# Kernel optimization log

Hardware: AMD Instinct MI355X
Metric: run time of the kernel (lower is better)

Reference implementation:

```python
import jax, jax.numpy as jnp
import numpy as np

WH, WW = 16, 16            # window size
NUM_HEADS = 8


def _relative_position_index(wh, ww):
    ch = jnp.arange(wh)
    cw = jnp.arange(ww)
    coords = jnp.stack(jnp.meshgrid(ch, cw, indexing='ij'))        # [2, wh, ww]
    coords = coords.reshape(2, -1)                                  # [2, N]
    rel = coords[:, :, None] - coords[:, None, :]                   # [2, N, N]
    rel = rel.transpose(1, 2, 0)                                    # [N, N, 2]
    idx = (rel[..., 0] + wh - 1) * (2 * ww - 1) + (rel[..., 1] + ww - 1)
    return idx                                                      # [N, N] int32


def setup_inputs() -> dict:
    key = jax.random.key(0)
    ks = jax.random.split(key, 7)
    B, N, C = 128, WH * WW, 512
    x = jax.random.normal(ks[0], (B, N, C), dtype=jnp.float32)
    y = jax.random.normal(ks[1], (B, N, C), dtype=jnp.float32)
    # Linear weights stored as [in, out]; init ~ standard scale
    q_w = jax.random.normal(ks[2], (C, C), dtype=jnp.float32) * (C ** -0.5)
    kv_w = jax.random.normal(ks[3], (C, 2 * C), dtype=jnp.float32) * (C ** -0.5)
    proj_w = jax.random.normal(ks[4], (C, C), dtype=jnp.float32) * (C ** -0.5)
    proj_b = jax.random.normal(ks[5], (C,), dtype=jnp.float32) * 0.01
    n_rel = (2 * WH - 1) * (2 * WW - 1)  # 961
    bias_table = jax.random.normal(ks[6], (n_rel, NUM_HEADS), dtype=jnp.float32) * 0.02
    return {"x": x, "y": y, "q_w": q_w, "kv_w": kv_w,
            "proj_w": proj_w, "proj_b": proj_b, "bias_table": bias_table}


def reference(x, y, q_w, kv_w, proj_w, proj_b, bias_table):
    B, N1, C = x.shape
    _, N2, _ = y.shape
    H = NUM_HEADS
    d = C // H
    scale = d ** -0.5

    q = (x @ q_w).reshape(B, N1, H, d).transpose(0, 2, 1, 3)        # [B,H,N1,d]
    kv = (y @ kv_w).reshape(B, N2, 2, H, d)
    k = kv[:, :, 0].transpose(0, 2, 1, 3)                           # [B,H,N2,d]
    v = kv[:, :, 1].transpose(0, 2, 1, 3)                           # [B,H,N2,d]

    attn = jnp.einsum('bhqd,bhkd->bhqk', q, k) * scale              # [B,H,N1,N2]

    idx = _relative_position_index(WH, WW)                          # [N, N]
    rel_bias = bias_table[idx.reshape(-1)].reshape(N1, N2, H)       # gather
    rel_bias = rel_bias.transpose(2, 0, 1)                          # [H,N1,N2]
    attn = attn + rel_bias[None]

    attn = jax.nn.softmax(attn, axis=-1)
    out = jnp.einsum('bhqk,bhkd->bhqd', attn, v)                    # [B,H,N1,d]
    out = out.transpose(0, 2, 1, 3).reshape(B, N1, C)
    out = out @ proj_w + proj_b
    return out
```

## Files before the change

kernel.cpp:

```cpp
#include <hip/hip_runtime.h>

typedef unsigned short u16;
typedef __attribute__((ext_vector_type(8))) short short8;
typedef __attribute__((ext_vector_type(4))) float floatx4;

__device__ __forceinline__ float bf2f(u16 v){
  union { unsigned int u; float f; } x; x.u = ((unsigned int)v) << 16; return x.f;
}
__device__ __forceinline__ u16 f2bf(float f){
  union { float f; unsigned int u; } x; x.f = f;
  unsigned int r = x.u + 0x7FFFu + ((x.u >> 16) & 1u);
  return (u16)(r >> 16);
}
__device__ __forceinline__ short8 cvt8(float4 f0, float4 f1){
  short8 v;
  v[0] = (short)f2bf(f0.x); v[1] = (short)f2bf(f0.y);
  v[2] = (short)f2bf(f0.z); v[3] = (short)f2bf(f0.w);
  v[4] = (short)f2bf(f1.x); v[5] = (short)f2bf(f1.y);
  v[6] = (short)f2bf(f1.z); v[7] = (short)f2bf(f1.w);
  return v;
}

__device__ __forceinline__ void async16(const void* g, void* l){
  __builtin_amdgcn_global_load_lds(
      (__attribute__((address_space(1))) unsigned int*)const_cast<void*>(g),
      (__attribute__((address_space(3))) unsigned int*)l, 16, 0, 0);
}

__global__ __launch_bounds__(256)
void conv_bf16(const float* __restrict__ in, u16* __restrict__ out, int n8){
  const int stride = gridDim.x * 256;
  for (int i = blockIdx.x * 256 + threadIdx.x; i < n8; i += stride){
    float4 f0 = ((const float4*)in)[(size_t)i * 2];
    float4 f1 = ((const float4*)in)[(size_t)i * 2 + 1];
    *(short8*)(out + (size_t)i * 8) = cvt8(f0, f1);
  }
}

__global__ void transpose_f32(const float* __restrict__ in, u16* __restrict__ out,
                              int R, int C){
  __shared__ u16 t[32][33];
  const int tx = threadIdx.x;
  const int c0 = blockIdx.x * 32, r0 = blockIdx.y * 32;
  for (int i = tx; i < 1024; i += 256){
    int r = i >> 5, c = i & 31;
    t[r][c] = f2bf(in[(size_t)(r0 + r) * C + c0 + c]);
  }
  __syncthreads();
  for (int i = tx; i < 1024; i += 256){
    int r = i >> 5, c = i & 31;
    out[(size_t)(c0 + r) * R + r0 + c] = t[c][r];
  }
}

__global__ void bias_expand(const float* __restrict__ table, u16* __restrict__ Bm){
  int i = blockIdx.x * 256 + threadIdx.x;
  int q = i >> 8, k = i & 255;
  int rh = (q >> 4) - (k >> 4) + 15;
  int rw = (q & 15) - (k & 15) + 15;
  int idx = rh * 31 + rw;
  #pragma unroll
  for (int h = 0; h < 8; h++) Bm[h * 65536 + i] = f2bf(table[(size_t)idx * 8 + h]);
}

template<int MODE, int GX>
__global__ __launch_bounds__(512, 2)
void gemm_bt(const u16* __restrict__ A, const u16* __restrict__ Bt,
             void* __restrict__ O0, u16* __restrict__ O1,
             const float* __restrict__ bias)
{
  __shared__ __align__(16) u16 As[3][256 * 64];
  __shared__ __align__(16) u16 Bs[3][128 * 64];
  const int tid  = threadIdx.x;
  const int lane = tid & 63, wave = tid >> 6;
  const int q16  = lane & 15, quad = lane >> 4;
  const int wr   = wave >> 1, wc = wave & 1;

  constexpr int NWG = 128 * GX;
  constexpr int CPX = NWG / 8;
  const int bid = blockIdx.x;
  const int swz = (bid & 7) * CPX + (bid >> 3);
  const int rowBase = (swz / GX) * 256;
  const int colBase = (swz % GX) * 128;

  const u16* Ap = A  + (size_t)rowBase * 512;
  const u16* Bp = Bt + (size_t)colBase * 512;

  floatx4 acc[4][4];
  #pragma unroll
  for (int i = 0; i < 4; i++)
    #pragma unroll
    for (int j = 0; j < 4; j++) acc[i][j] = floatx4{0.f, 0.f, 0.f, 0.f};

  int sra[4], sca[4];
  #pragma unroll
  for (int j = 0; j < 4; j++){
    int p = tid + j * 512;
    sra[j] = p >> 3;
    sca[j] = ((p & 7) ^ (sra[j] & 7)) * 8;
  }

  auto STAGE = [&](int slot, int kt){
    #pragma unroll
    for (int j = 0; j < 4; j++){
      u16* d = &As[slot][(size_t)(j * 512 + wave * 64) * 8];
      async16(Ap + (size_t)sra[j] * 512 + kt * 64 + sca[j], d);
    }
    #pragma unroll
    for (int j = 0; j < 2; j++){
      u16* d = &Bs[slot][(size_t)(j * 512 + wave * 64) * 8];
      async16(Bp + (size_t)sra[j] * 512 + kt * 64 + sca[j], d);
    }
  };

  STAGE(0, 0);
  STAGE(1, 1);

  #pragma unroll
  for (int kt = 0; kt < 8; kt++){
    const int cs = kt % 3;
    if (kt < 7) asm volatile("s_waitcnt vmcnt(6)" ::: "memory");
    else        asm volatile("s_waitcnt vmcnt(0)" ::: "memory");
    __builtin_amdgcn_s_barrier();
    __builtin_amdgcn_sched_barrier(0);
    if (kt + 2 < 8) STAGE((kt + 2) % 3, kt + 2);
    __builtin_amdgcn_sched_barrier(0);

    __builtin_amdgcn_s_setprio(1);
    #pragma unroll
    for (int kk = 0; kk < 2; kk++){
      short8 af[4], bfr[4];
      #pragma unroll
      for (int mt = 0; mt < 4; mt++){
        int r  = wr * 64 + mt * 16 + q16;
        int ph = ((kk * 4 + quad) ^ (r & 7)) * 8;
        af[mt] = *(const short8*)(&As[cs][r * 64 + ph]);
      }
      #pragma unroll
      for (int nt = 0; nt < 4; nt++){
        int r  = wc * 64 + nt * 16 + q16;
        int ph = ((kk * 4 + quad) ^ (r & 7)) * 8;
        bfr[nt] = *(const short8*)(&Bs[cs][r * 64 + ph]);
      }
      #pragma unroll
      for (int mt = 0; mt < 4; mt++)
        #pragma unroll
        for (int nt = 0; nt < 4; nt++)
          acc[mt][nt] = __builtin_amdgcn_mfma_f32_16x16x32_bf16(
              af[mt], bfr[nt], acc[mt][nt], 0, 0, 0);
    }
    __builtin_amdgcn_s_setprio(0);
  }

  #pragma unroll
  for (int mt = 0; mt < 4; mt++){
    #pragma unroll
    for (int nt = 0; nt < 4; nt++){
      const floatx4 v = acc[mt][nt];
      const int col = colBase + wc * 64 + nt * 16 + q16;
      #pragma unroll
      for (int r = 0; r < 4; r++){
        const int row = rowBase + wr * 64 + mt * 16 + quad * 4 + r;
        if (MODE == 0){
          int bb = row >> 8, n = row & 255, hh = col >> 6, dd = col & 63;
          ((u16*)O0)[(((size_t)(bb * 8 + hh)) * 256 + n) * 64 + dd] = f2bf(v[r]);
        } else if (MODE == 1){
          int bb = row >> 8, key = row & 255;
          int two = col >> 9, hh = (col >> 6) & 7, dd = col & 63;
          if (two == 0)
            ((u16*)O0)[(((size_t)(bb * 8 + hh)) * 256 + key) * 64 + dd] = f2bf(v[r]);
          else
            O1[(((size_t)(bb * 8 + hh)) * 64 + dd) * 256 + key] = f2bf(v[r]);
        } else {
          ((float*)O0)[(size_t)row * 512 + col] = v[r] + bias[col];
        }
      }
    }
  }
}

__global__ __launch_bounds__(256)
void attn_kernel(const u16* __restrict__ Qb, const u16* __restrict__ Kb,
                 const u16* __restrict__ Vtb, const u16* __restrict__ Bm,
                 u16* __restrict__ Ob)
{
  constexpr int PS = 264;
  __shared__ __align__(16) u16 Vs[64 * PS];
  __shared__ __align__(16) u16 Pss[4 * 16 * PS];
  const int bh = blockIdx.x;
  const int b = bh >> 3, h = bh & 7;
  const u16* Qp = Qb  + (size_t)bh * 256 * 64;
  const u16* Kp = Kb  + (size_t)bh * 256 * 64;
  const u16* Vp = Vtb + (size_t)bh * 64 * 256;
  const u16* Bp = Bm  + (size_t)h * 65536;
  const int tid = threadIdx.x;
  const int lane = tid & 63, wave = tid >> 6;
  const int q16 = lane & 15, quad = lane >> 4;
  u16* Pw = Pss + wave * 16 * PS;

  for (int i = tid; i < 64 * 32; i += 256){
    int dd = i >> 5, kc = (i & 31) * 8;
    *(short8*)(Vs + dd * PS + kc) = *(const short8*)(Vp + dd * 256 + kc);
  }
  __syncthreads();

  for (int chunk = 0; chunk < 4; chunk++){
    const int qbase = wave * 64 + chunk * 16;
    const short8 qa0 = *(const short8*)(Qp + (qbase + q16) * 64 + quad * 8);
    const short8 qa1 = *(const short8*)(Qp + (qbase + q16) * 64 + 32 + quad * 8);

    floatx4 acc[16];
    #pragma unroll
    for (int kt = 0; kt < 16; kt++) acc[kt] = floatx4{0.f, 0.f, 0.f, 0.f};
    #pragma unroll
    for (int kt = 0; kt < 16; kt++){
      const u16* kr = Kp + (kt * 16 + q16) * 64 + quad * 8;
      acc[kt] = __builtin_amdgcn_mfma_f32_16x16x32_bf16(
          qa0, *(const short8*)(kr), acc[kt], 0, 0, 0);
      acc[kt] = __builtin_amdgcn_mfma_f32_16x16x32_bf16(
          qa1, *(const short8*)(kr + 32), acc[kt], 0, 0, 0);
    }

    floatx4 mrow = {-3e38f, -3e38f, -3e38f, -3e38f};
    #pragma unroll
    for (int kt = 0; kt < 16; kt++){
      const u16* bb = Bp + (qbase + quad * 4) * 256 + kt * 16 + q16;
      floatx4 v = acc[kt];
      #pragma unroll
      for (int r = 0; r < 4; r++){
        float t = v[r] * 0.125f + bf2f(bb[(size_t)r * 256]);
        v[r] = t;
        mrow[r] = fmaxf(mrow[r], t);
      }
      acc[kt] = v;
    }
    #pragma unroll
    for (int off = 1; off < 16; off <<= 1){
      #pragma unroll
      for (int r = 0; r < 4; r++)
        mrow[r] = fmaxf(mrow[r], __shfl_xor(mrow[r], off, 64));
    }

    floatx4 lrow = {0.f, 0.f, 0.f, 0.f};
    #pragma unroll
    for (int kt = 0; kt < 16; kt++){
      floatx4 v = acc[kt];
      #pragma unroll
      for (int r = 0; r < 4; r++){
        float e = exp2f((v[r] - mrow[r]) * 1.4426950408889634f);
        v[r] = e;
        lrow[r] += e;
      }
      #pragma unroll
      for (int r = 0; r < 4; r++)
        Pw[(quad * 4 + r) * PS + kt * 16 + q16] = f2bf(v[r]);
    }
    #pragma unroll
    for (int off = 1; off < 16; off <<= 1){
      #pragma unroll
      for (int r = 0; r < 4; r++) lrow[r] += __shfl_xor(lrow[r], off, 64);
    }

    __syncthreads();

    short8 pa[8];
    #pragma unroll
    for (int k2 = 0; k2 < 8; k2++)
      pa[k2] = *(const short8*)(Pw + q16 * PS + k2 * 32 + quad * 8);
    floatx4 o[4];
    #pragma unroll
    for (int nt = 0; nt < 4; nt++) o[nt] = floatx4{0.f, 0.f, 0.f, 0.f};
    #pragma unroll
    for (int nt = 0; nt < 4; nt++)
      #pragma unroll
      for (int k2 = 0; k2 < 8; k2++){
        const short8 vb = *(const short8*)(Vs + (nt * 16 + q16) * PS + k2 * 32 + quad * 8);
        o[nt] = __builtin_amdgcn_mfma_f32_16x16x32_bf16(pa[k2], vb, o[nt], 0, 0, 0);
      }

    floatx4 rl;
    #pragma unroll
    for (int r = 0; r < 4; r++) rl[r] = 1.0f / lrow[r];
    #pragma unroll
    for (int nt = 0; nt < 4; nt++)
      #pragma unroll
      for (int r = 0; r < 4; r++){
        int q = qbase + quad * 4 + r;
        Ob[((size_t)(b * 256 + q)) * 512 + h * 64 + nt * 16 + q16] =
            f2bf(o[nt][r] * rl[r]);
      }
  }
}

extern "C" void kernel_launch(void* const* d_in, const int* in_sizes, int n_in,
                              void* d_out, int out_size, void* d_ws, size_t ws_size,
                              hipStream_t stream)
{
  (void)in_sizes; (void)n_in; (void)out_size; (void)ws_size;
  const float* x      = (const float*)d_in[0];
  const float* y      = (const float*)d_in[1];
  const float* q_w    = (const float*)d_in[2];
  const float* kv_w   = (const float*)d_in[3];
  const float* proj_w = (const float*)d_in[4];
  const float* proj_b = (const float*)d_in[5];
  const float* btab   = (const float*)d_in[6];
  float* out = (float*)d_out;
  char* w = (char*)d_ws;

  u16* Qb   = (u16*)(w);
  u16* Kb   = (u16*)(w + 33554432);
  u16* Vtb  = (u16*)(w + 67108864);
  u16* Ab   = (u16*)(w + 100663296);
  u16* qwT  = (u16*)(w + 134217728);
  u16* kvwT = (u16*)(w + 134742016);
  u16* pwT  = (u16*)(w + 135790592);
  u16* Bm   = (u16*)(w + 136314880);

  transpose_f32<<<dim3(16, 16), 256, 0, stream>>>(q_w,    qwT,  512, 512);
  transpose_f32<<<dim3(32, 16), 256, 0, stream>>>(kv_w,   kvwT, 512, 1024);
  transpose_f32<<<dim3(16, 16), 256, 0, stream>>>(proj_w, pwT,  512, 512);
  bias_expand<<<dim3(256), 256, 0, stream>>>(btab, Bm);

  conv_bf16<<<dim3(2048), 256, 0, stream>>>(x, Ab, 2097152);
  gemm_bt<0, 4><<<dim3(512),  512, 0, stream>>>(Ab, qwT,  Qb,  nullptr, nullptr);
  conv_bf16<<<dim3(2048), 256, 0, stream>>>(y, Ab, 2097152);
  gemm_bt<1, 8><<<dim3(1024), 512, 0, stream>>>(Ab, kvwT, Kb,  Vtb,     nullptr);
  attn_kernel<<<dim3(1024), 256, 0, stream>>>(Qb, Kb, Vtb, Bm, Ab);
  gemm_bt<2, 4><<<dim3(512),  512, 0, stream>>>(Ab, pwT,  out, nullptr, proj_b);
}
```

Measured before the change: 410.8 us.

## Fold bias into MFMA accumulator init and drop V LDS staging in attention

The relative-position bias is now stored transposed and pre-scaled by 8. Each lane loads it as a packed 4-element vector to initialise the QK^T accumulators, which replaces the per-element strided bias loads in the softmax loop. V is no longer staged in shared memory; it is read directly from global memory as the MFMA B operand. This removes the initial copy and both block-wide barriers, since each wave only uses its own P buffer. The change also adds s_setprio around the MFMA loops and a launch-bounds occupancy hint, trading lower LDS use for more global/L2 traffic on V.

```diff
diff --git a/kernel.cpp b/kernel.cpp
--- a/kernel.cpp
+++ b/kernel.cpp
@@ -3,6 +3,7 @@
 typedef unsigned short u16;
 typedef __attribute__((ext_vector_type(8))) short short8;
 typedef __attribute__((ext_vector_type(4))) float floatx4;
+typedef __attribute__((ext_vector_type(4))) unsigned short ushort4v;
 
 __device__ __forceinline__ float bf2f(u16 v){
   union { unsigned int u; float f; } x; x.u = ((unsigned int)v) << 16; return x.f;
@@ -55,12 +56,13 @@
 
 __global__ void bias_expand(const float* __restrict__ table, u16* __restrict__ Bm){
   int i = blockIdx.x * 256 + threadIdx.x;
-  int q = i >> 8, k = i & 255;
+  int k = i >> 8, q = i & 255;
   int rh = (q >> 4) - (k >> 4) + 15;
   int rw = (q & 15) - (k & 15) + 15;
   int idx = rh * 31 + rw;
   #pragma unroll
-  for (int h = 0; h < 8; h++) Bm[h * 65536 + i] = f2bf(table[(size_t)idx * 8 + h]);
+  for (int h = 0; h < 8; h++)
+    Bm[h * 65536 + i] = f2bf(8.0f * table[(size_t)idx * 8 + h]);
 }
 
 template<int MODE, int GX>
@@ -179,13 +181,12 @@
   }
 }
 
-__global__ __launch_bounds__(256)
+__global__ __launch_bounds__(256, 4)
 void attn_kernel(const u16* __restrict__ Qb, const u16* __restrict__ Kb,
                  const u16* __restrict__ Vtb, const u16* __restrict__ Bm,
                  u16* __restrict__ Ob)
 {
   constexpr int PS = 264;
-  __shared__ __align__(16) u16 Vs[64 * PS];
   __shared__ __align__(16) u16 Pss[4 * 16 * PS];
   const int bh = blockIdx.x;
   const int b = bh >> 3, h = bh & 7;
@@ -198,12 +199,6 @@
   const int q16 = lane & 15, quad = lane >> 4;
   u16* Pw = Pss + wave * 16 * PS;
 
-  for (int i = tid; i < 64 * 32; i += 256){
-    int dd = i >> 5, kc = (i & 31) * 8;
-    *(short8*)(Vs + dd * PS + kc) = *(const short8*)(Vp + dd * 256 + kc);
-  }
-  __syncthreads();
-
   for (int chunk = 0; chunk < 4; chunk++){
     const int qbase = wave * 64 + chunk * 16;
     const short8 qa0 = *(const short8*)(Qp + (qbase + q16) * 64 + quad * 8);
@@ -211,7 +206,16 @@
 
     floatx4 acc[16];
     #pragma unroll
-    for (int kt = 0; kt < 16; kt++) acc[kt] = floatx4{0.f, 0.f, 0.f, 0.f};
+    for (int kt = 0; kt < 16; kt++){
+      ushort4v bv = *(const ushort4v*)(Bp + (size_t)(kt * 16 + q16) * 256
+                                          + qbase + quad * 4);
+      floatx4 a;
+      a[0] = bf2f(bv[0]); a[1] = bf2f(bv[1]);
+      a[2] = bf2f(bv[2]); a[3] = bf2f(bv[3]);
+      acc[kt] = a;
+    }
+
+    __builtin_amdgcn_s_setprio(1);
     #pragma unroll
     for (int kt = 0; kt < 16; kt++){
       const u16* kr = Kp + (kt * 16 + q16) * 64 + quad * 8;
@@ -220,15 +224,15 @@
       acc[kt] = __builtin_amdgcn_mfma_f32_16x16x32_bf16(
           qa1, *(const short8*)(kr + 32), acc[kt], 0, 0, 0);
     }
+    __builtin_amdgcn_s_setprio(0);
 
     floatx4 mrow = {-3e38f, -3e38f, -3e38f, -3e38f};
     #pragma unroll
     for (int kt = 0; kt < 16; kt++){
-      const u16* bb = Bp + (qbase + quad * 4) * 256 + kt * 16 + q16;
       floatx4 v = acc[kt];
       #pragma unroll
       for (int r = 0; r < 4; r++){
-        float t = v[r] * 0.125f + bf2f(bb[(size_t)r * 256]);
+        float t = v[r] * 0.125f;
         v[r] = t;
         mrow[r] = fmaxf(mrow[r], t);
       }
@@ -261,22 +265,26 @@
       for (int r = 0; r < 4; r++) lrow[r] += __shfl_xor(lrow[r], off, 64);
     }
 
-    __syncthreads();
-
-    short8 pa[8];
-    #pragma unroll
-    for (int k2 = 0; k2 < 8; k2++)
-      pa[k2] = *(const short8*)(Pw + q16 * PS + k2 * 32 + quad * 8);
     floatx4 o[4];
     #pragma unroll
     for (int nt = 0; nt < 4; nt++) o[nt] = floatx4{0.f, 0.f, 0.f, 0.f};
     #pragma unroll
-    for (int nt = 0; nt < 4; nt++)
-      #pragma unroll
-      for (int k2 = 0; k2 < 8; k2++){
-        const short8 vb = *(const short8*)(Vs + (nt * 16 + q16) * PS + k2 * 32 + quad * 8);
-        o[nt] = __builtin_amdgcn_mfma_f32_16x16x32_bf16(pa[k2], vb, o[nt], 0, 0, 0);
-      }
+    for (int half = 0; half < 2; half++){
+      short8 pa[4];
+      #pragma unroll
+      for (int k2 = 0; k2 < 4; k2++)
+        pa[k2] = *(const short8*)(Pw + q16 * PS + (half * 4 + k2) * 32 + quad * 8);
+      __builtin_amdgcn_s_setprio(1);
+      #pragma unroll
+      for (int nt = 0; nt < 4; nt++)
+        #pragma unroll
+        for (int k2 = 0; k2 < 4; k2++){
+          const short8 vb = *(const short8*)(Vp + (size_t)(nt * 16 + q16) * 256
+                                                + (half * 4 + k2) * 32 + quad * 8);
+          o[nt] = __builtin_amdgcn_mfma_f32_16x16x32_bf16(pa[k2], vb, o[nt], 0, 0, 0);
+        }
+      __builtin_amdgcn_s_setprio(0);
+    }
 
     floatx4 rl;
     #pragma unroll
```

New measurement: 623.6 us. +51.8%, slower.
